# Kernel tuning notes

Measured on AMD Instinct MI355X. Metric: run time of the kernel, lower is better.

Reference implementation:

```python
import jax, jax.numpy as jnp
import numpy as np

HEADS = 8
DIM_HEAD = 128
SCALE = DIM_HEAD ** -0.5
EPS = 1e-5


def layer_norm(t, w, b):
    mu = t.mean(-1, keepdims=True)
    var = ((t - mu) ** 2).mean(-1, keepdims=True)
    return (t - mu) * jax.lax.rsqrt(var + EPS) * w + b


def setup_inputs() -> dict:
    key = jax.random.key(0)
    ks = jax.random.split(key, 8)
    b, n, dim = 4, 1024, 1024
    inner = HEADS * DIM_HEAD  # 1024
    w = 0.02
    return {
        "x": jax.random.normal(ks[0], (b, n, dim), jnp.float32),
        "cond_info": jax.random.normal(ks[1], (b, n, dim), jnp.float32),
        "ref": jax.random.normal(ks[2], (b, n, dim), jnp.float32),
        "ln_w": jnp.ones((dim,), jnp.float32),
        "ln_b": jnp.zeros((dim,), jnp.float32),
        "cln_w": jnp.ones((dim,), jnp.float32),
        "cln_b": jnp.zeros((dim,), jnp.float32),
        "Wk": jax.random.normal(ks[3], (3 * dim, inner), jnp.float32) * w,
        "Wv": jax.random.normal(ks[4], (2 * dim, inner), jnp.float32) * w,
        "Wo": jax.random.normal(ks[5], (inner, dim), jnp.float32) * w,
        "bo": jnp.zeros((dim,), jnp.float32),
        "th_w": jax.random.normal(ks[6], (HEADS, HEADS), jnp.float32) * 0.3,
        "cth_w": jax.random.normal(ks[7], (HEADS, HEADS), jnp.float32) * 0.3,
    }


def reference(x, cond_info, ref, ln_w, ln_b, cln_w, cln_b, Wk, Wv, Wo, bo, th_w, cth_w):
    b, n, _ = x.shape
    h, d = HEADS, DIM_HEAD
    xn = layer_norm(x, ln_w, ln_b)
    rn = layer_norm(ref, ln_w, ln_b)
    cn = layer_norm(cond_info, cln_w, cln_b)
    # projections (y_to_q output is unused in the original forward; omitted)
    cond = jnp.concatenate([xn, cn, rn], axis=-1) @ Wk   # [b, n, h*d]
    refv = jnp.concatenate([xn, rn], axis=-1) @ Wv       # [b, n, h*d]
    split = lambda t: t.reshape(b, n, h, d).transpose(0, 2, 1, 3)  # b h n d
    cond, refv = split(cond), split(refv)
    sim = jnp.einsum('bhid,bhjd->bhij', cond, refv) * SCALE
    attn = jax.nn.softmax(sim, axis=-1)           # row softmax
    context_attn = jax.nn.softmax(sim, axis=-2)   # column softmax
    # talking heads: 1x1 conv over head dim, weight [out_h, in_h]
    attn = jnp.einsum('gh,bhij->bgij', th_w, attn)
    context_attn = jnp.einsum('gh,bhij->bgij', cth_w, context_attn)
    out = jnp.einsum('bhij,bhjd->bhid', attn, refv)
    context_out = jnp.einsum('bhji,bhjd->bhid', context_attn, cond)
    merge = lambda t: t.transpose(0, 2, 1, 3).reshape(b, n, h * d)
    out = merge(out) @ Wo + bo
    context_out = merge(context_out)
    return out, context_out
```

## Files before the change

kernel.cpp:

```cpp
#include <hip/hip_runtime.h>
#include <hip/hip_bf16.h>
#include <stdint.h>

typedef unsigned short u16;
typedef __attribute__((ext_vector_type(8))) short bf16x8;
typedef __attribute__((ext_vector_type(4))) float f32x4;

#define HEADS 8
#define DHEAD 128
#define NSEQ 1024
#define BATCH 4
#define DIM 1024
#define ATT_SCALE 0.088388347648318447f

static __device__ __forceinline__ float bf2f(u16 u){
  union { unsigned int i; float f; } c; c.i = ((unsigned int)u) << 16; return c.f;
}
static __device__ __forceinline__ u16 f2bf(float f){
  union { float f; unsigned int i; } c; c.f = f;
  unsigned int x = c.i;
  return (u16)((x + 0x7fffu + ((x >> 16) & 1u)) >> 16);
}

static __device__ __forceinline__ void gload_lds16(const void* g, void* l){
  __builtin_amdgcn_global_load_lds((__attribute__((address_space(1))) void*)(g),
                                   (__attribute__((address_space(3))) void*)(l),
                                   16, 0, 0);
}

__global__ __launch_bounds__(256)
void ln3_kernel(const float* __restrict__ x, const float* __restrict__ ref,
                const float* __restrict__ cinfo,
                const float* __restrict__ ln_w, const float* __restrict__ ln_b,
                const float* __restrict__ cln_w, const float* __restrict__ cln_b,
                u16* __restrict__ xn, u16* __restrict__ rn, u16* __restrict__ cn)
{
  const int z = blockIdx.y;
  const float* src = (z==0) ? x : (z==1) ? ref : cinfo;
  const float* w   = (z==2) ? cln_w : ln_w;
  const float* b   = (z==2) ? cln_b : ln_b;
  u16* out         = (z==0) ? xn : (z==1) ? rn : cn;

  const int row = blockIdx.x;
  const int t = threadIdx.x;
  const float* xr = src + (size_t)row * DIM;
  float4 v4 = *(const float4*)(xr + t*4);
  float v[4] = {v4.x, v4.y, v4.z, v4.w};
  float s = v[0]+v[1]+v[2]+v[3];
  __shared__ float red[256];
  red[t] = s; __syncthreads();
  for (int o=128;o;o>>=1){ if (t<o) red[t]+=red[t+o]; __syncthreads(); }
  const float mean = red[0] * (1.0f/DIM);
  __syncthreads();
  s = 0.f;
#pragma unroll
  for (int i=0;i<4;i++){ float d = v[i]-mean; s += d*d; }
  red[t] = s; __syncthreads();
  for (int o=128;o;o>>=1){ if (t<o) red[t]+=red[t+o]; __syncthreads(); }
  const float rstd = rsqrtf(red[0]*(1.0f/DIM) + 1e-5f);
  float4 w4 = *(const float4*)(w + t*4);
  float4 b4 = *(const float4*)(b + t*4);
  float wv[4] = {w4.x, w4.y, w4.z, w4.w};
  float bv[4] = {b4.x, b4.y, b4.z, b4.w};
  union { uint2 u; u16 s[4]; } ov;
#pragma unroll
  for (int i=0;i<4;i++)
    ov.s[i] = f2bf((v[i]-mean)*rstd*wv[i] + bv[i]);
  *(uint2*)(out + (size_t)row*DIM + t*4) = ov.u;
}

__global__ __launch_bounds__(256)
void wcvt_kernel(const float* __restrict__ Wk, const float* __restrict__ Wv,
                 const float* __restrict__ Wo,
                 u16* __restrict__ WkT, u16* __restrict__ WvT, u16* __restrict__ WoT)
{
  const int z = blockIdx.z;
  const int K = (z==0) ? 3072 : (z==1) ? 2048 : 1024;
  if ((int)blockIdx.x*32 >= K) return;
  const float* W = (z==0) ? Wk : (z==1) ? Wv : Wo;
  u16* WT = (z==0) ? WkT : (z==1) ? WvT : WoT;
  __shared__ float tile[32][33];
  const int k0 = blockIdx.x*32, n0 = blockIdx.y*32;
  const int t = threadIdx.x, tc = t&31, tr = t>>5;
#pragma unroll
  for (int p=0;p<4;p++)
    tile[tr+p*8][tc] = W[(size_t)(k0+tr+p*8)*DIM + n0+tc];
  __syncthreads();
#pragma unroll
  for (int p=0;p<4;p++)
    WT[(size_t)(n0+tr+p*8)*K + k0+tc] = f2bf(tile[tc][tr+p*8]);
}

__global__ __launch_bounds__(256)
void gemmsk2_kernel(const u16* __restrict__ xn, const u16* __restrict__ cn,
                    const u16* __restrict__ rn,
                    const u16* __restrict__ WkT, const u16* __restrict__ WvT,
                    float* __restrict__ Pc, float* __restrict__ Pr)
{
  __shared__ __attribute__((aligned(16))) u16 sA[2][4096];
  __shared__ __attribute__((aligned(16))) u16 sB[2][4096];
  const int t = threadIdx.x;
  const int bid = blockIdx.x;
  const int swz = (bid & 7)*160 + (bid >> 3);
  const bool condside = swz < 768;
  const int w = condside ? swz : swz - 768;
  const int s = w >> 8;
  const int rem = w & 255;
  const int x = rem & 7, y = rem >> 3;
  const int m0 = y*128, n0 = x*128;
  const u16* A = condside ? (s==0 ? xn : (s==1 ? cn : rn))
                          : (s==0 ? xn : rn);
  const u16* B = (condside ? WkT : WvT) + s*1024;
  const int ldb = condside ? 3072 : 2048;
  float* P = (condside ? Pc : Pr) + (size_t)s*4194304;

  const int wave = t>>6, lane = t&63;
  const int wm = (wave>>1)*64, wn = (wave&1)*64;
  const int lm = lane&15, q = lane>>4;

  const f32x4 zero4 = {0.f,0.f,0.f,0.f};
  f32x4 acc[4][4];
#pragma unroll
  for (int i=0;i<4;i++)
#pragma unroll
    for (int j=0;j<4;j++) acc[i][j] = zero4;

  const int arowblk = wave*32;

  auto issueA = [&](int kt, int buf){
    const int kg = kt<<5;
#pragma unroll
    for (int rr=0; rr<2; ++rr){
      const int rb = arowblk + rr*16;
      gload_lds16(A + (size_t)(m0+rb+lm)*1024 + (kg + q*8), &sA[buf][rb*32]);
    }
  };
  auto issueB = [&](int kt, int buf){
    const int kg = kt<<5;
#pragma unroll
    for (int rr=0; rr<2; ++rr){
      const int rb = arowblk + rr*16;
      gload_lds16(B + (size_t)(n0+rb+lm)*ldb + (kg + q*8), &sB[buf][rb*32]);
    }
  };

  issueA(0, 0); issueB(0, 0);

  int cur = 0;
  for (int kt=0; kt<32; ++kt){
    __syncthreads();
    if (kt+1 < 32){
      issueA(kt+1, cur^1);
      issueB(kt+1, cur^1);
    }
    bf16x8 af[4], bfr[4];
#pragma unroll
    for (int f=0; f<4; ++f){
      af[f]  = *(const bf16x8*)&sA[cur][((wm>>4)+f)*512 + lane*8];
      bfr[f] = *(const bf16x8*)&sB[cur][((wn>>4)+f)*512 + lane*8];
    }
#pragma unroll
    for (int fm=0; fm<4; ++fm)
#pragma unroll
      for (int fn=0; fn<4; ++fn)
        acc[fm][fn] = __builtin_amdgcn_mfma_f32_16x16x32_bf16(af[fm], bfr[fn], acc[fm][fn], 0, 0, 0);
    cur ^= 1;
  }

#pragma unroll
  for (int fm=0; fm<4; ++fm){
#pragma unroll
    for (int fn=0; fn<4; ++fn){
#pragma unroll
      for (int r=0; r<4; ++r){
        const int m = m0 + wm + fm*16 + q*4 + r;
        const int n = n0 + wn + fn*16 + lm;
        P[(size_t)m*1024 + n] = acc[fm][fn][r];
      }
    }
  }
}

__global__ __launch_bounds__(256)
void redsk2_kernel(const float* __restrict__ Pc, const float* __restrict__ Pr,
                   u16* __restrict__ cond, u16* __restrict__ refv)
{
  const int bid = blockIdx.x;
  const bool condside = bid < 4096;
  const int idx = (condside ? bid : bid-4096)*256 + threadIdx.x;
  const float4* P4 = (const float4*)(condside ? Pc : Pr);
  float4 a = P4[idx];
  float4 b = P4[idx + 1048576];
  float4 o;
  o.x = a.x + b.x; o.y = a.y + b.y; o.z = a.z + b.z; o.w = a.w + b.w;
  if (condside){
    float4 c = P4[idx + 2097152];
    o.x += c.x; o.y += c.y; o.z += c.z; o.w += c.w;
  }
  const int nlin = idx*4;
  const int m = nlin >> 10, n = nlin & 1023;
  u16* dst = condside ? cond : refv;
  union { uint2 u; u16 s[4]; } ov;
  ov.s[0] = f2bf(o.x); ov.s[1] = f2bf(o.y);
  ov.s[2] = f2bf(o.z); ov.s[3] = f2bf(o.w);
  *(uint2*)&dst[((size_t)((m>>10)*HEADS + (n>>7))*NSEQ + (m&1023))*DHEAD + (n&127)] = ov.u;
}

template<int BK>
__global__ __launch_bounds__(256)
void gemm_kernel(const u16* __restrict__ A0, const u16* __restrict__ A1,
                 const u16* __restrict__ A2, const u16* __restrict__ A0b,
                 const u16* __restrict__ A1b,
                 const u16* __restrict__ B1, const u16* __restrict__ B2,
                 void* __restrict__ Cv, void* __restrict__ Cv2,
                 const float* __restrict__ bias,
                 int K1, int K2, int lda, int ldb1, int ldb2, int ldc,
                 long a_plane, long b_plane, long c_plane,
                 int epi1, int epi2, int z_split, float alpha)
{
  constexpr int SUBS = BK/32;
  __shared__ __attribute__((aligned(16))) u16 sA[2][SUBS*4096];
  __shared__ __attribute__((aligned(16))) u16 sB[2][SUBS*4096];
  const int t = threadIdx.x;
  const int m0 = blockIdx.y*128, n0 = blockIdx.x*128;
  const int zz = blockIdx.z;
  const bool side = (zz >= z_split);
  const int z = side ? (zz - z_split) : zz;
  const u16* a0 = (side ? A0b : A0) + (size_t)z*a_plane;
  const u16* a1 = (side ? A1b : A1) + (size_t)z*a_plane;
  const u16* a2 = A2 + (size_t)z*a_plane;
  const u16* bB = (side ? B2 : B1) + (size_t)z*b_plane;
  void* Cp = side ? Cv2 : Cv;
  const int EPI = side ? epi2 : epi1;
  const int K   = side ? K2 : K1;
  const int ldb = side ? ldb2 : ldb1;

  const int wave = t>>6, lane = t&63;
  const int wm = (wave>>1)*64, wn = (wave&1)*64;
  const int lm = lane&15, q = lane>>4;

  const f32x4 zero4 = {0.f,0.f,0.f,0.f};
  f32x4 acc[4][4];
#pragma unroll
  for (int i=0;i<4;i++)
#pragma unroll
    for (int j=0;j<4;j++) acc[i][j] = zero4;

  const int arowblk = wave*32;

  const int KT = K / BK;

  auto issueA = [&](int kt, int buf){
    const int kg = kt*BK, seg = kg>>10, ka = kg&1023;
    const u16* Ap = (seg==0) ? a0 : (seg==1 ? a1 : a2);
#pragma unroll
    for (int sub=0; sub<SUBS; ++sub)
#pragma unroll
      for (int rr=0; rr<2; ++rr){
        const int rb = arowblk + rr*16;
        gload_lds16(Ap + (size_t)(m0+rb+lm)*lda + (ka + sub*32 + q*8),
                    &sA[buf][sub*4096 + rb*32]);
      }
  };
  auto issueB = [&](int kt, int buf){
    const int kg = kt*BK;
#pragma unroll
    for (int sub=0; sub<SUBS; ++sub)
#pragma unroll
      for (int rr=0; rr<2; ++rr){
        const int rb = arowblk + rr*16;
        gload_lds16(bB + (size_t)(n0+rb+lm)*ldb + (kg + sub*32 + q*8),
                    &sB[buf][sub*4096 + rb*32]);
      }
  };

  issueA(0, 0);
  issueB(0, 0);

  int cur = 0;
  for (int kt=0; kt<KT; ++kt){
    __syncthreads();
    if (kt+1 < KT){
      issueA(kt+1, cur^1);
      issueB(kt+1, cur^1);
    }
#pragma unroll
    for (int sub=0; sub<SUBS; ++sub){
      bf16x8 af[4], bfr[4];
#pragma unroll
      for (int f=0; f<4; ++f){
        af[f]  = *(const bf16x8*)&sA[cur][sub*4096 + ((wm>>4)+f)*512 + lane*8];
        bfr[f] = *(const bf16x8*)&sB[cur][sub*4096 + ((wn>>4)+f)*512 + lane*8];
      }
#pragma unroll
      for (int fm=0; fm<4; ++fm)
#pragma unroll
        for (int fn=0; fn<4; ++fn)
          acc[fm][fn] = __builtin_amdgcn_mfma_f32_16x16x32_bf16(af[fm], bfr[fn], acc[fm][fn], 0, 0, 0);
    }
    cur ^= 1;
  }

#pragma unroll
  for (int fm=0; fm<4; ++fm){
#pragma unroll
    for (int fn=0; fn<4; ++fn){
#pragma unroll
      for (int r=0; r<4; ++r){
        const int m = m0 + wm + fm*16 + q*4 + r;
        const int n = n0 + wn + fn*16 + lm;
        float val = acc[fm][fn][r] * alpha;
        if (EPI == 0){
          ((u16*)Cp)[(size_t)z*c_plane + (size_t)m*ldc + n] = f2bf(val);
        } else if (EPI == 1){
          ((u16*)Cp)[((size_t)(z>>3)*NSEQ + m)*DIM + (size_t)(z&7)*DHEAD + n] = f2bf(val);
        } else if (EPI == 2){
          ((float*)Cp)[(size_t)m*ldc + n] = val + bias[n];
        } else if (EPI == 3){
          ((u16*)Cp)[(size_t)(((m>>10)*HEADS + (n>>7))*NSEQ + (m&1023))*DHEAD + (n&127)] = f2bf(val);
        } else {
          ((float*)Cp)[((size_t)(z>>3)*NSEQ + m)*DIM + (size_t)(z&7)*DHEAD + n] = val;
        }
      }
    }
  }
}

__global__ __launch_bounds__(256)
void gemm8_kernel(const u16* __restrict__ A, const u16* __restrict__ B,
                  float* __restrict__ P)
{
  __shared__ __attribute__((aligned(16))) u16 sA[2][4096];
  __shared__ __attribute__((aligned(16))) u16 sB[2][4096];
  const int t = threadIdx.x;
  const int bid = blockIdx.x;
  const int w = (bid & 7)*128 + (bid >> 3);
  const int x = w & 7;
  const int y = (w >> 3) & 31;
  const int s = w >> 8;
  const int m0 = y*128, n0 = x*128, k0 = s*256;

  const int wave = t>>6, lane = t&63;
  const int wm = (wave>>1)*64, wn = (wave&1)*64;
  const int lm = lane&15, q = lane>>4;

  const f32x4 zero4 = {0.f,0.f,0.f,0.f};
  f32x4 acc[4][4];
#pragma unroll
  for (int i=0;i<4;i++)
#pragma unroll
    for (int j=0;j<4;j++) acc[i][j] = zero4;

  const int arowblk = wave*32;

  auto issueA = [&](int kt, int buf){
    const int kg = k0 + (kt<<5);
#pragma unroll
    for (int rr=0; rr<2; ++rr){
      const int rb = arowblk + rr*16;
      gload_lds16(A + (size_t)(m0+rb+lm)*1024 + (kg + q*8), &sA[buf][rb*32]);
    }
  };
  auto issueB = [&](int kt, int buf){
    const int kg = k0 + (kt<<5);
#pragma unroll
    for (int rr=0; rr<2; ++rr){
      const int rb = arowblk + rr*16;
      gload_lds16(B + (size_t)(n0+rb+lm)*1024 + (kg + q*8), &sB[buf][rb*32]);
    }
  };

  issueA(0, 0); issueB(0, 0);

  int cur = 0;
  for (int kt=0; kt<8; ++kt){
    __syncthreads();
    if (kt+1 < 8){
      issueA(kt+1, cur^1);
      issueB(kt+1, cur^1);
    }
    bf16x8 af[4], bfr[4];
#pragma unroll
    for (int f=0; f<4; ++f){
      af[f]  = *(const bf16x8*)&sA[cur][((wm>>4)+f)*512 + lane*8];
      bfr[f] = *(const bf16x8*)&sB[cur][((wn>>4)+f)*512 + lane*8];
    }
#pragma unroll
    for (int fm=0; fm<4; ++fm)
#pragma unroll
      for (int fn=0; fn<4; ++fn)
        acc[fm][fn] = __builtin_amdgcn_mfma_f32_16x16x32_bf16(af[fm], bfr[fn], acc[fm][fn], 0, 0, 0);
    cur ^= 1;
  }

  float* Pp = P + (size_t)s*4194304;
#pragma unroll
  for (int fm=0; fm<4; ++fm){
#pragma unroll
    for (int fn=0; fn<4; ++fn){
#pragma unroll
      for (int r=0; r<4; ++r){
        const int m = m0 + wm + fm*16 + q*4 + r;
        const int n = n0 + wn + fn*16 + lm;
        Pp[(size_t)m*1024 + n] = acc[fm][fn][r];
      }
    }
  }
}

__global__ __launch_bounds__(256)
void red8_kernel(const float* __restrict__ P, const float* __restrict__ bias,
                 float* __restrict__ out)
{
  const int idx = blockIdx.x*256 + threadIdx.x;
  const float4* P4 = (const float4*)P;
  float4 a = P4[idx];
  float4 b = P4[idx + 1048576];
  float4 c = P4[idx + 2097152];
  float4 d = P4[idx + 3145728];
  float4 bb = ((const float4*)bias)[idx & 255];
  float4 o;
  o.x = a.x + b.x + c.x + d.x + bb.x;
  o.y = a.y + b.y + c.y + d.y + bb.y;
  o.z = a.z + b.z + c.z + d.z + bb.z;
  o.w = a.w + b.w + c.w + d.w + bb.w;
  ((float4*)out)[idx] = o;
}

__global__ __launch_bounds__(256)
void transpose2_kernel(const u16* __restrict__ cond, const u16* __restrict__ refv,
                       u16* __restrict__ condT, u16* __restrict__ refvT)
{
  __shared__ u16 tile[32][33];
  const int zz = blockIdx.z;
  const u16* X = (zz < 32) ? cond : refv;
  u16* XT      = (zz < 32) ? condT : refvT;
  const int z = zz & 31;
  const int i0 = blockIdx.y*32, d0 = blockIdx.x*32;
  const int t = threadIdx.x;
  const int tc = t & 31, tr = t >> 5;
  const u16* Xp = X + (size_t)z*NSEQ*DHEAD;
#pragma unroll
  for (int p=0;p<4;p++){
    int i = tr + p*8;
    tile[i][tc] = Xp[(size_t)(i0+i)*DHEAD + d0 + tc];
  }
  __syncthreads();
  u16* Op = XT + (size_t)z*DHEAD*NSEQ;
#pragma unroll
  for (int p=0;p<4;p++){
    int d = tr + p*8;
    Op[(size_t)(d0+d)*NSEQ + i0 + tc] = tile[tc][d];
  }
}

__global__ __launch_bounds__(256)
void stats_kernel(const u16* __restrict__ sim,
                  float* __restrict__ rmax, float* __restrict__ rrcp,
                  float* __restrict__ cmax, float* __restrict__ crcp)
{
  __shared__ float smx[4][64], ssm[4][64];
  if (blockIdx.x < 8192){
    const int wave = threadIdx.x >> 6, lane = threadIdx.x & 63;
    const int row = blockIdx.x*4 + wave;
    const u16* sr = sim + (size_t)row * NSEQ;
    float v[16]; float m = -1e30f;
#pragma unroll
    for (int c=0;c<16;c++){ v[c] = bf2f(sr[lane + c*64]); m = fmaxf(m, v[c]); }
#pragma unroll
    for (int off=32; off; off>>=1) m = fmaxf(m, __shfl_xor(m, off));
    float s = 0.f;
#pragma unroll
    for (int c=0;c<16;c++) s += __expf(v[c]-m);
#pragma unroll
    for (int off=32; off; off>>=1) s += __shfl_xor(s, off);
    if (lane == 0){ rmax[row] = m; rrcp[row] = 1.0f/s; }
  } else {
    const int t = threadIdx.x;
    const int jl = t & 63, slice = t >> 6;
    const int c = (blockIdx.x - 8192)*64 + jl;
    const int bh = c >> 10, j = c & 1023;
    const u16* sp = sim + (size_t)bh*NSEQ*NSEQ + j + (size_t)(slice*256)*NSEQ;
    float m0=-1e30f, m1=-1e30f, m2=-1e30f, m3=-1e30f;
    for (int i=0;i<256;i+=4){
      m0 = fmaxf(m0, bf2f(sp[(size_t)(i  )*NSEQ]));
      m1 = fmaxf(m1, bf2f(sp[(size_t)(i+1)*NSEQ]));
      m2 = fmaxf(m2, bf2f(sp[(size_t)(i+2)*NSEQ]));
      m3 = fmaxf(m3, bf2f(sp[(size_t)(i+3)*NSEQ]));
    }
    smx[slice][jl] = fmaxf(fmaxf(m0,m1), fmaxf(m2,m3));
    __syncthreads();
    const float M = fmaxf(fmaxf(smx[0][jl], smx[1][jl]),
                          fmaxf(smx[2][jl], smx[3][jl]));
    float s0=0.f, s1=0.f, s2=0.f, s3=0.f;
    for (int i=0;i<256;i+=4){
      s0 += __expf(bf2f(sp[(size_t)(i  )*NSEQ]) - M);
      s1 += __expf(bf2f(sp[(size_t)(i+1)*NSEQ]) - M);
      s2 += __expf(bf2f(sp[(size_t)(i+2)*NSEQ]) - M);
      s3 += __expf(bf2f(sp[(size_t)(i+3)*NSEQ]) - M);
    }
    ssm[slice][jl] = s0+s1+s2+s3;
    __syncthreads();
    if (slice == 0){
      float S = ssm[0][jl] + ssm[1][jl] + ssm[2][jl] + ssm[3][jl];
      cmax[c] = M; crcp[c] = 1.0f/S;
    }
  }
}

__global__ __launch_bounds__(256)
void mix_kernel(u16* simam,
                const float* __restrict__ rmax, const float* __restrict__ rrcp,
                const float* __restrict__ cmax, const float* __restrict__ crcp,
                const float* __restrict__ thw, const float* __restrict__ cthw,
                u16* __restrict__ cmT)
{
  __shared__ float s_th[64], s_cth[64];
  __shared__ u16 s_cm[8][32][33];
  const int t = threadIdx.x;
  if (t < 64){ s_th[t] = thw[t]; s_cth[t] = cthw[t]; }
  __syncthreads();
  const int b = blockIdx.z, i0 = blockIdx.y*32, j0 = blockIdx.x*32;
  const int tj = t & 31, ti = t >> 5;
  for (int p=0;p<4;p++){
    const int i = ti + p*8;
    float a[8], c[8];
#pragma unroll
    for (int h=0;h<8;h++){
      const int bh = b*8 + h;
      const float v = bf2f(simam[((size_t)bh*NSEQ + (i0+i))*NSEQ + j0 + tj]);
      a[h] = __expf(v - rmax[(size_t)bh*NSEQ + i0+i]) * rrcp[(size_t)bh*NSEQ + i0+i];
      c[h] = __expf(v - cmax[(size_t)bh*NSEQ + j0+tj]) * crcp[(size_t)bh*NSEQ + j0+tj];
    }
#pragma unroll
    for (int g=0;g<8;g++){
      float sa = 0.f, sc = 0.f;
#pragma unroll
      for (int h=0;h<8;h++){ sa += s_th[g*8+h]*a[h]; sc += s_cth[g*8+h]*c[h]; }
      simam[((size_t)(b*8+g)*NSEQ + (i0+i))*NSEQ + j0 + tj] = f2bf(sa);
      s_cm[g][i][tj] = f2bf(sc);
    }
  }
  __syncthreads();
#pragma unroll
  for (int g=0;g<8;g++){
#pragma unroll
    for (int p=0;p<4;p++){
      const int j = ti + p*8;
      cmT[((size_t)(b*8+g)*NSEQ + (j0+j))*NSEQ + i0 + tj] = s_cm[g][tj][j];
    }
  }
}

extern "C" void kernel_launch(void* const* d_in, const int* in_sizes, int n_in,
                              void* d_out, int out_size, void* d_ws, size_t ws_size,
                              hipStream_t stream)
{
  const float* x     = (const float*)d_in[0];
  const float* cinfo = (const float*)d_in[1];
  const float* ref   = (const float*)d_in[2];
  const float* ln_w  = (const float*)d_in[3];
  const float* ln_b  = (const float*)d_in[4];
  const float* cln_w = (const float*)d_in[5];
  const float* cln_b = (const float*)d_in[6];
  const float* Wk    = (const float*)d_in[7];
  const float* Wv    = (const float*)d_in[8];
  const float* Wo    = (const float*)d_in[9];
  const float* bo    = (const float*)d_in[10];
  const float* thw   = (const float*)d_in[11];
  const float* cthw  = (const float*)d_in[12];
  float* out = (float*)d_out;

  char* ws = (char*)d_ws;
  u16* xn    = (u16*)(ws + 0);
  u16* cn    = (u16*)(ws + 8388608);
  u16* rn    = (u16*)(ws + 16777216);
  u16* cond  = (u16*)(ws + 25165824);
  u16* refv  = (u16*)(ws + 33554432);
  u16* condT = (u16*)(ws + 41943040);
  u16* refvT = (u16*)(ws + 50331648);
  u16* sim   = (u16*)(ws + 58720256);
  u16* cmT   = (u16*)(ws + 125829120);
  u16* WkT   = (u16*)(ws + 192937984);
  u16* WvT   = (u16*)(ws + 199229440);
  u16* WoT   = (u16*)(ws + 203423744);
  float* rmax = (float*)(ws + 8388608);
  float* rrcp = (float*)(ws + 8388608 + 131072);
  float* cmax = (float*)(ws + 8388608 + 262144);
  float* crcp = (float*)(ws + 8388608 + 393216);
  u16* out_pre = (u16*)(ws + 0);

  ln3_kernel<<<dim3(4096,3), 256, 0, stream>>>(x, ref, cinfo, ln_w, ln_b,
                                               cln_w, cln_b, xn, rn, cn);

  wcvt_kernel<<<dim3(96,32,3), 256, 0, stream>>>(Wk, Wv, Wo, WkT, WvT, WoT);

  gemmsk2_kernel<<<1280, 256, 0, stream>>>(xn, cn, rn, WkT, WvT,
                                           (float*)sim, (float*)cmT);
  redsk2_kernel<<<8192, 256, 0, stream>>>((const float*)sim, (const float*)cmT,
                                          cond, refv);

  transpose2_kernel<<<dim3(4,32,64), 256, 0, stream>>>(cond, refv, condT, refvT);

  gemm_kernel<32><<<dim3(8,8,32), 256, 0, stream>>>(
      cond, cond, cond, cond, cond, refv, refv, sim, sim, nullptr,
      DHEAD, DHEAD, DHEAD, DHEAD, DHEAD, NSEQ,
      (long)NSEQ*DHEAD, (long)NSEQ*DHEAD, (long)NSEQ*NSEQ, 0, 0, 1000000, ATT_SCALE);

  stats_kernel<<<8704, 256, 0, stream>>>(sim, rmax, rrcp, cmax, crcp);

  mix_kernel<<<dim3(32,32,4), 256, 0, stream>>>(sim, rmax, rrcp, cmax, crcp, thw, cthw, cmT);

  gemm_kernel<64><<<dim3(1,8,64), 256, 0, stream>>>(
      sim, sim, sim, cmT, cmT, refvT, condT, out_pre, out + (size_t)BATCH*NSEQ*DIM, nullptr,
      1024, 1024, NSEQ, NSEQ, NSEQ, 0,
      (long)NSEQ*NSEQ, (long)DHEAD*NSEQ, 0, 1, 4, 32, 1.0f);

  gemm8_kernel<<<1024, 256, 0, stream>>>(out_pre, WoT, (float*)sim);
  red8_kernel<<<4096, 256, 0, stream>>>((const float*)sim, bo, out);
}
```

Before: 524.9 us.

## Fuse softmax partial stats into QK GEMM epilogue and drop split-K projection

```diff
diff --git a/kernel.cpp b/kernel.cpp
--- a/kernel.cpp
+++ b/kernel.cpp
@@ -89,121 +89,6 @@
 #pragma unroll
   for (int p=0;p<4;p++)
     WT[(size_t)(n0+tr+p*8)*K + k0+tc] = f2bf(tile[tc][tr+p*8]);
-}
-
-__global__ __launch_bounds__(256)
-void gemmsk2_kernel(const u16* __restrict__ xn, const u16* __restrict__ cn,
-                    const u16* __restrict__ rn,
-                    const u16* __restrict__ WkT, const u16* __restrict__ WvT,
-                    float* __restrict__ Pc, float* __restrict__ Pr)
-{
-  __shared__ __attribute__((aligned(16))) u16 sA[2][4096];
-  __shared__ __attribute__((aligned(16))) u16 sB[2][4096];
-  const int t = threadIdx.x;
-  const int bid = blockIdx.x;
-  const int swz = (bid & 7)*160 + (bid >> 3);
-  const bool condside = swz < 768;
-  const int w = condside ? swz : swz - 768;
-  const int s = w >> 8;
-  const int rem = w & 255;
-  const int x = rem & 7, y = rem >> 3;
-  const int m0 = y*128, n0 = x*128;
-  const u16* A = condside ? (s==0 ? xn : (s==1 ? cn : rn))
-                          : (s==0 ? xn : rn);
-  const u16* B = (condside ? WkT : WvT) + s*1024;
-  const int ldb = condside ? 3072 : 2048;
-  float* P = (condside ? Pc : Pr) + (size_t)s*4194304;
-
-  const int wave = t>>6, lane = t&63;
-  const int wm = (wave>>1)*64, wn = (wave&1)*64;
-  const int lm = lane&15, q = lane>>4;
-
-  const f32x4 zero4 = {0.f,0.f,0.f,0.f};
-  f32x4 acc[4][4];
-#pragma unroll
-  for (int i=0;i<4;i++)
-#pragma unroll
-    for (int j=0;j<4;j++) acc[i][j] = zero4;
-
-  const int arowblk = wave*32;
-
-  auto issueA = [&](int kt, int buf){
-    const int kg = kt<<5;
-#pragma unroll
-    for (int rr=0; rr<2; ++rr){
-      const int rb = arowblk + rr*16;
-      gload_lds16(A + (size_t)(m0+rb+lm)*1024 + (kg + q*8), &sA[buf][rb*32]);
-    }
-  };
-  auto issueB = [&](int kt, int buf){
-    const int kg = kt<<5;
-#pragma unroll
-    for (int rr=0; rr<2; ++rr){
-      const int rb = arowblk + rr*16;
-      gload_lds16(B + (size_t)(n0+rb+lm)*ldb + (kg + q*8), &sB[buf][rb*32]);
-    }
-  };
-
-  issueA(0, 0); issueB(0, 0);
-
-  int cur = 0;
-  for (int kt=0; kt<32; ++kt){
-    __syncthreads();
-    if (kt+1 < 32){
-      issueA(kt+1, cur^1);
-      issueB(kt+1, cur^1);
-    }
-    bf16x8 af[4], bfr[4];
-#pragma unroll
-    for (int f=0; f<4; ++f){
-      af[f]  = *(const bf16x8*)&sA[cur][((wm>>4)+f)*512 + lane*8];
-      bfr[f] = *(const bf16x8*)&sB[cur][((wn>>4)+f)*512 + lane*8];
-    }
-#pragma unroll
-    for (int fm=0; fm<4; ++fm)
-#pragma unroll
-      for (int fn=0; fn<4; ++fn)
-        acc[fm][fn] = __builtin_amdgcn_mfma_f32_16x16x32_bf16(af[fm], bfr[fn], acc[fm][fn], 0, 0, 0);
-    cur ^= 1;
-  }
-
-#pragma unroll
-  for (int fm=0; fm<4; ++fm){
-#pragma unroll
-    for (int fn=0; fn<4; ++fn){
-#pragma unroll
-      for (int r=0; r<4; ++r){
-        const int m = m0 + wm + fm*16 + q*4 + r;
-        const int n = n0 + wn + fn*16 + lm;
-        P[(size_t)m*1024 + n] = acc[fm][fn][r];
-      }
-    }
-  }
-}
-
-__global__ __launch_bounds__(256)
-void redsk2_kernel(const float* __restrict__ Pc, const float* __restrict__ Pr,
-                   u16* __restrict__ cond, u16* __restrict__ refv)
-{
-  const int bid = blockIdx.x;
-  const bool condside = bid < 4096;
-  const int idx = (condside ? bid : bid-4096)*256 + threadIdx.x;
-  const float4* P4 = (const float4*)(condside ? Pc : Pr);
-  float4 a = P4[idx];
-  float4 b = P4[idx + 1048576];
-  float4 o;
-  o.x = a.x + b.x; o.y = a.y + b.y; o.z = a.z + b.z; o.w = a.w + b.w;
-  if (condside){
-    float4 c = P4[idx + 2097152];
-    o.x += c.x; o.y += c.y; o.z += c.z; o.w += c.w;
-  }
-  const int nlin = idx*4;
-  const int m = nlin >> 10, n = nlin & 1023;
-  u16* dst = condside ? cond : refv;
-  union { uint2 u; u16 s[4]; } ov;
-  ov.s[0] = f2bf(o.x); ov.s[1] = f2bf(o.y);
-  ov.s[2] = f2bf(o.z); ov.s[3] = f2bf(o.w);
-  *(uint2*)&dst[((size_t)((m>>10)*HEADS + (n>>7))*NSEQ + (m&1023))*DHEAD + (n&127)] = ov.u;
 }
 
 template<int BK>
@@ -327,6 +212,155 @@
 }
 
 __global__ __launch_bounds__(256)
+void gemmqk_kernel(const u16* __restrict__ cond, const u16* __restrict__ refv,
+                   u16* __restrict__ sim,
+                   float* __restrict__ RP, float* __restrict__ RS,
+                   float* __restrict__ CP, float* __restrict__ CS)
+{
+  __shared__ __attribute__((aligned(16))) u16 sA[2][4096];
+  __shared__ __attribute__((aligned(16))) u16 sB[2][4096];
+  const int t = threadIdx.x;
+  const int m0 = blockIdx.y*128, n0 = blockIdx.x*128;
+  const int z = blockIdx.z;
+  const u16* A = cond + (size_t)z*NSEQ*DHEAD;
+  const u16* B = refv + (size_t)z*NSEQ*DHEAD;
+
+  const int wave = t>>6, lane = t&63;
+  const int wm = (wave>>1)*64, wn = (wave&1)*64;
+  const int lm = lane&15, q = lane>>4;
+
+  const f32x4 zero4 = {0.f,0.f,0.f,0.f};
+  f32x4 acc[4][4];
+#pragma unroll
+  for (int i=0;i<4;i++)
+#pragma unroll
+    for (int j=0;j<4;j++) acc[i][j] = zero4;
+
+  const int arowblk = wave*32;
+
+  auto issueA = [&](int kt, int buf){
+    const int kg = kt<<5;
+#pragma unroll
+    for (int rr=0; rr<2; ++rr){
+      const int rb = arowblk + rr*16;
+      gload_lds16(A + (size_t)(m0+rb+lm)*DHEAD + (kg + q*8), &sA[buf][rb*32]);
+    }
+  };
+  auto issueB = [&](int kt, int buf){
+    const int kg = kt<<5;
+#pragma unroll
+    for (int rr=0; rr<2; ++rr){
+      const int rb = arowblk + rr*16;
+      gload_lds16(B + (size_t)(n0+rb+lm)*DHEAD + (kg + q*8), &sB[buf][rb*32]);
+    }
+  };
+
+  issueA(0, 0); issueB(0, 0);
+
+  int cur = 0;
+  for (int kt=0; kt<4; ++kt){
+    __syncthreads();
+    if (kt+1 < 4){
+      issueA(kt+1, cur^1);
+      issueB(kt+1, cur^1);
+    }
+    bf16x8 af[4], bfr[4];
+#pragma unroll
+    for (int f=0; f<4; ++f){
+      af[f]  = *(const bf16x8*)&sA[cur][((wm>>4)+f)*512 + lane*8];
+      bfr[f] = *(const bf16x8*)&sB[cur][((wn>>4)+f)*512 + lane*8];
+    }
+#pragma unroll
+    for (int fm=0; fm<4; ++fm)
+#pragma unroll
+      for (int fn=0; fn<4; ++fn)
+        acc[fm][fn] = __builtin_amdgcn_mfma_f32_16x16x32_bf16(af[fm], bfr[fn], acc[fm][fn], 0, 0, 0);
+    cur ^= 1;
+  }
+
+#pragma unroll
+  for (int fm=0; fm<4; ++fm){
+#pragma unroll
+    for (int fn=0; fn<4; ++fn){
+#pragma unroll
+      for (int r=0; r<4; ++r){
+        const int m = m0 + wm + fm*16 + q*4 + r;
+        const int n = n0 + wn + fn*16 + lm;
+        const u16 bv = f2bf(acc[fm][fn][r] * ATT_SCALE);
+        sim[((size_t)z*NSEQ + m)*NSEQ + n] = bv;
+        acc[fm][fn][r] = bf2f(bv);
+      }
+    }
+  }
+
+  const int xg = blockIdx.x*2 + (wn>>6);
+#pragma unroll
+  for (int fm=0; fm<4; ++fm){
+#pragma unroll
+    for (int r=0; r<4; ++r){
+      float rm = fmaxf(fmaxf(acc[fm][0][r], acc[fm][1][r]),
+                       fmaxf(acc[fm][2][r], acc[fm][3][r]));
+#pragma unroll
+      for (int msk=1; msk<16; msk<<=1) rm = fmaxf(rm, __shfl_xor(rm, msk));
+      float rs = __expf(acc[fm][0][r]-rm) + __expf(acc[fm][1][r]-rm)
+               + __expf(acc[fm][2][r]-rm) + __expf(acc[fm][3][r]-rm);
+#pragma unroll
+      for (int msk=1; msk<16; msk<<=1) rs += __shfl_xor(rs, msk);
+      if (lm == 0){
+        const int m = m0 + wm + fm*16 + q*4 + r;
+        RP[((size_t)z*NSEQ + m)*16 + xg] = rm;
+        RS[((size_t)z*NSEQ + m)*16 + xg] = rs;
+      }
+    }
+  }
+
+  const int yg = blockIdx.y*2 + (wm>>6);
+#pragma unroll
+  for (int fn=0; fn<4; ++fn){
+    float cm = -1e30f;
+#pragma unroll
+    for (int fm=0; fm<4; ++fm)
+#pragma unroll
+      for (int r=0; r<4; ++r) cm = fmaxf(cm, acc[fm][fn][r]);
+    cm = fmaxf(cm, __shfl_xor(cm, 16));
+    cm = fmaxf(cm, __shfl_xor(cm, 32));
+    float cs = 0.f;
+#pragma unroll
+    for (int fm=0; fm<4; ++fm)
+#pragma unroll
+      for (int r=0; r<4; ++r) cs += __expf(acc[fm][fn][r]-cm);
+    cs += __shfl_xor(cs, 16);
+    cs += __shfl_xor(cs, 32);
+    if (q == 0){
+      const int n = n0 + wn + fn*16 + lm;
+      CP[((size_t)z*NSEQ + n)*16 + yg] = cm;
+      CS[((size_t)z*NSEQ + n)*16 + yg] = cs;
+    }
+  }
+}
+
+__global__ __launch_bounds__(256)
+void redstats_kernel(const float* __restrict__ RP, const float* __restrict__ RS,
+                     const float* __restrict__ CP, const float* __restrict__ CS,
+                     float* __restrict__ rmax, float* __restrict__ rrcp,
+                     float* __restrict__ cmax, float* __restrict__ crcp)
+{
+  const int gid = blockIdx.x*256 + threadIdx.x;
+  const bool isrow = gid < 32768;
+  const int item = isrow ? gid : gid - 32768;
+  const float* P = isrow ? RP : CP;
+  const float* S = isrow ? RS : CS;
+  float M = -1e30f;
+#pragma unroll
+  for (int g=0; g<16; g++) M = fmaxf(M, P[(size_t)item*16 + g]);
+  float s = 0.f;
+#pragma unroll
+  for (int g=0; g<16; g++) s += S[(size_t)item*16 + g] * __expf(P[(size_t)item*16 + g] - M);
+  if (isrow){ rmax[item] = M; rrcp[item] = 1.0f/s; }
+  else      { cmax[item] = M; crcp[item] = 1.0f/s; }
+}
+
+__global__ __launch_bounds__(256)
 void gemm8_kernel(const u16* __restrict__ A, const u16* __restrict__ B,
                   float* __restrict__ P)
 {
@@ -451,60 +485,6 @@
   for (int p=0;p<4;p++){
     int d = tr + p*8;
     Op[(size_t)(d0+d)*NSEQ + i0 + tc] = tile[tc][d];
-  }
-}
-
-__global__ __launch_bounds__(256)
-void stats_kernel(const u16* __restrict__ sim,
-                  float* __restrict__ rmax, float* __restrict__ rrcp,
-                  float* __restrict__ cmax, float* __restrict__ crcp)
-{
-  __shared__ float smx[4][64], ssm[4][64];
-  if (blockIdx.x < 8192){
-    const int wave = threadIdx.x >> 6, lane = threadIdx.x & 63;
-    const int row = blockIdx.x*4 + wave;
-    const u16* sr = sim + (size_t)row * NSEQ;
-    float v[16]; float m = -1e30f;
-#pragma unroll
-    for (int c=0;c<16;c++){ v[c] = bf2f(sr[lane + c*64]); m = fmaxf(m, v[c]); }
-#pragma unroll
-    for (int off=32; off; off>>=1) m = fmaxf(m, __shfl_xor(m, off));
-    float s = 0.f;
-#pragma unroll
-    for (int c=0;c<16;c++) s += __expf(v[c]-m);
-#pragma unroll
-    for (int off=32; off; off>>=1) s += __shfl_xor(s, off);
-    if (lane == 0){ rmax[row] = m; rrcp[row] = 1.0f/s; }
-  } else {
-    const int t = threadIdx.x;
-    const int jl = t & 63, slice = t >> 6;
-    const int c = (blockIdx.x - 8192)*64 + jl;
-    const int bh = c >> 10, j = c & 1023;
-    const u16* sp = sim + (size_t)bh*NSEQ*NSEQ + j + (size_t)(slice*256)*NSEQ;
-    float m0=-1e30f, m1=-1e30f, m2=-1e30f, m3=-1e30f;
-    for (int i=0;i<256;i+=4){
-      m0 = fmaxf(m0, bf2f(sp[(size_t)(i  )*NSEQ]));
-      m1 = fmaxf(m1, bf2f(sp[(size_t)(i+1)*NSEQ]));
-      m2 = fmaxf(m2, bf2f(sp[(size_t)(i+2)*NSEQ]));
-      m3 = fmaxf(m3, bf2f(sp[(size_t)(i+3)*NSEQ]));
-    }
-    smx[slice][jl] = fmaxf(fmaxf(m0,m1), fmaxf(m2,m3));
-    __syncthreads();
-    const float M = fmaxf(fmaxf(smx[0][jl], smx[1][jl]),
-                          fmaxf(smx[2][jl], smx[3][jl]));
-    float s0=0.f, s1=0.f, s2=0.f, s3=0.f;
-    for (int i=0;i<256;i+=4){
-      s0 += __expf(bf2f(sp[(size_t)(i  )*NSEQ]) - M);
-      s1 += __expf(bf2f(sp[(size_t)(i+1)*NSEQ]) - M);
-      s2 += __expf(bf2f(sp[(size_t)(i+2)*NSEQ]) - M);
-      s3 += __expf(bf2f(sp[(size_t)(i+3)*NSEQ]) - M);
-    }
-    ssm[slice][jl] = s0+s1+s2+s3;
-    __syncthreads();
-    if (slice == 0){
-      float S = ssm[0][jl] + ssm[1][jl] + ssm[2][jl] + ssm[3][jl];
-      cmax[c] = M; crcp[c] = 1.0f/S;
-    }
   }
 }
 
@@ -584,10 +564,14 @@
   u16* WkT   = (u16*)(ws + 192937984);
   u16* WvT   = (u16*)(ws + 199229440);
   u16* WoT   = (u16*)(ws + 203423744);
-  float* rmax = (float*)(ws + 8388608);
-  float* rrcp = (float*)(ws + 8388608 + 131072);
-  float* cmax = (float*)(ws + 8388608 + 262144);
-  float* crcp = (float*)(ws + 8388608 + 393216);
+  float* RP = (float*)(ws + 8388608);
+  float* RS = (float*)(ws + 8388608 + 2097152);
+  float* CP = (float*)(ws + 8388608 + 4194304);
+  float* CS = (float*)(ws + 8388608 + 6291456);
+  float* rmax = (float*)(ws + 16777216);
+  float* rrcp = (float*)(ws + 16777216 + 131072);
+  float* cmax = (float*)(ws + 16777216 + 262144);
+  float* crcp = (float*)(ws + 16777216 + 393216);
   u16* out_pre = (u16*)(ws + 0);
 
   ln3_kernel<<<dim3(4096,3), 256, 0, stream>>>(x, ref, cinfo, ln_w, ln_b,
@@ -595,19 +579,14 @@
 
   wcvt_kernel<<<dim3(96,32,3), 256, 0, stream>>>(Wk, Wv, Wo, WkT, WvT, WoT);
 
-  gemmsk2_kernel<<<1280, 256, 0, stream>>>(xn, cn, rn, WkT, WvT,
-                                           (float*)sim, (float*)cmT);
-  redsk2_kernel<<<8192, 256, 0, stream>>>((const float*)sim, (const float*)cmT,
-                                          cond, refv);
+  gemm_kernel<64><<<dim3(8,32,2), 256, 0, stream>>>(
+      xn, cn, rn, xn, rn, WkT, WvT, cond, refv, nullptr,
+      3072, 2048, DIM, 3072, 2048, 0, 0, 0, 0, 3, 3, 1, 1.0f);
 
   transpose2_kernel<<<dim3(4,32,64), 256, 0, stream>>>(cond, refv, condT, refvT);
 
-  gemm_kernel<32><<<dim3(8,8,32), 256, 0, stream>>>(
-      cond, cond, cond, cond, cond, refv, refv, sim, sim, nullptr,
-      DHEAD, DHEAD, DHEAD, DHEAD, DHEAD, NSEQ,
-      (long)NSEQ*DHEAD, (long)NSEQ*DHEAD, (long)NSEQ*NSEQ, 0, 0, 1000000, ATT_SCALE);
-
-  stats_kernel<<<8704, 256, 0, stream>>>(sim, rmax, rrcp, cmax, crcp);
+  gemmqk_kernel<<<dim3(8,8,32), 256, 0, stream>>>(cond, refv, sim, RP, RS, CP, CS);
+  redstats_kernel<<<256, 256, 0, stream>>>(RP, RS, CP, CS, rmax, rrcp, cmax, crcp);
 
   mix_kernel<<<dim3(32,32,4), 256, 0, stream>>>(sim, rmax, rrcp, cmax, crcp, thw, cthw, cmT);
 
```

After: 447.4 us. 14.8% less time.
